# Kernel optimization log

Hardware: AMD Instinct MI355X
Metric: run time of the kernel (lower is better)

Reference implementation:

```python
import jax, jax.numpy as jnp
import numpy as np

B, T, I, H, C = 8192, 28, 28, 128, 10


def setup_inputs() -> dict:
    key = jax.random.key(0)
    ks = jax.random.split(key, 7)
    s_ih = 1.0 / np.sqrt(H)
    return {
        "x": jax.random.normal(ks[0], (B, T, I), dtype=jnp.float32),
        "W_ih": jax.random.normal(ks[1], (4 * H, I), dtype=jnp.float32) * s_ih,
        "W_hh": jax.random.normal(ks[2], (4 * H, H), dtype=jnp.float32) * s_ih,
        "b_ih": jax.random.normal(ks[3], (4 * H,), dtype=jnp.float32) * s_ih,
        "b_hh": jax.random.normal(ks[4], (4 * H,), dtype=jnp.float32) * s_ih,
        "W_fc": jax.random.normal(ks[5], (C, H), dtype=jnp.float32) * s_ih,
        "b_fc": jnp.zeros((C,), dtype=jnp.float32),
    }


def reference(x, W_ih, W_hh, b_ih, b_hh, W_fc, b_fc):
    # x: [B, T, I]. PyTorch LSTM gate order: i, f, g, o.
    b = b_ih + b_hh  # [4H]
    # Precompute input projections for all timesteps: [T, B, 4H]
    x_proj = jnp.einsum("bti,gi->tbg", x, W_ih) + b
    h0 = jnp.zeros((x.shape[0], H), dtype=x.dtype)
    c0 = jnp.zeros_like(h0)

    def step(carry, xp_t):
        h, c = carry
        gates = xp_t + h @ W_hh.T  # [B, 4H]
        i_g, f_g, g_g, o_g = jnp.split(gates, 4, axis=-1)
        i_g = jax.nn.sigmoid(i_g)
        f_g = jax.nn.sigmoid(f_g)
        g_g = jnp.tanh(g_g)
        o_g = jax.nn.sigmoid(o_g)
        c = f_g * c + i_g * g_g
        h = o_g * jnp.tanh(c)
        return (h, c), None

    (h_last, _), _ = jax.lax.scan(step, (h0, c0), x_proj)
    # outputs[:, -1, :] == final hidden state; fc + relu
    return jax.nn.relu(h_last @ W_fc.T + b_fc)
```

## Files before the change

kernel.cpp:

```cpp
#include <hip/hip_runtime.h>
#include <math.h>

typedef __attribute__((ext_vector_type(8))) _Float16 half8;
typedef __attribute__((ext_vector_type(4))) _Float16 half4;
typedef __attribute__((ext_vector_type(4))) float    f32x4;

#define TSTEPS 28
#define IDIM   28
#define HDIM   128
#define NKC    5
#define TILE_B 16
#define CDIM   10

#if __has_builtin(__builtin_amdgcn_exp2f)
#define EXP2F(x) __builtin_amdgcn_exp2f(x)
#else
#define EXP2F(x) exp2f(x)
#endif
#if __has_builtin(__builtin_amdgcn_rcpf)
#define RCPF(x) __builtin_amdgcn_rcpf(x)
#else
#define RCPF(x) (1.0f / (x))
#endif

#define NLOG2E (-1.44269504f)
#define P2LOG2E (2.88539008f)

__global__ __launch_bounds__(256) void pack_w(const float* __restrict__ Wih,
                                              const float* __restrict__ Whh,
                                              _Float16* __restrict__ P) {
    int e = blockIdx.x * 256 + threadIdx.x;
    if (e >= NKC * 4 * 8 * 64 * 8) return;
    int j  = e & 7;
    int ln = (e >> 3) & 63;
    int w  = (e >> 9) & 7;
    int t  = (e >> 12) & 3;
    int kc = e >> 14;
    int k  = kc * 32 + ((ln >> 4) << 3) + j;
    int u  = w * 16 + (ln & 15);
    int g  = t * HDIM + u;
    float v = 0.f;
    if (k < HDIM)              v = Whh[g * HDIM + k];
    else if (k < HDIM + IDIM)  v = Wih[g * IDIM + (k - HDIM)];
    float sc = (t == 2) ? P2LOG2E : NLOG2E;
    P[e] = (_Float16)(v * sc);
}

__global__ __launch_bounds__(512, 4) void lstm_kernel(
    const float* __restrict__ x,
    const _Float16* __restrict__ P,
    const float* __restrict__ b_ih, const float* __restrict__ b_hh,
    const float* __restrict__ Wfc,
    const float* __restrict__ b_fc,
    float* __restrict__ out)
{
    __shared__ __align__(16) _Float16 frag[2][NKC][64][8];
    __shared__ __align__(16) _Float16 Plds[4][8][64][8];
    __shared__ __align__(16) float hplain[TILE_B][HDIM + 4];

    const int tid = threadIdx.x;
    const int l   = tid & 63;
    const int w   = tid >> 6;
    const int b0  = blockIdx.x * TILE_B;
    const int u   = w * 16 + (l & 15);

    {
        const float4* P4 = (const float4*)P;
        float4* dst = (float4*)Plds;
        #pragma unroll
        for (int q = 0; q < 4; ++q)
            dst[tid + q * 512] = P4[8192 + tid + q * 512];
    }
    half8 breg[4][4];
    {
        const half8* Pp = (const half8*)P;
        #pragma unroll
        for (int kc = 0; kc < 4; ++kc)
            #pragma unroll
            for (int t4 = 0; t4 < 4; ++t4)
                breg[t4][kc] = Pp[((kc * 4 + t4) * 8 + w) * 64 + l];
    }
    float biasv[4];
    #pragma unroll
    for (int t4 = 0; t4 < 4; ++t4) {
        float sc = (t4 == 2) ? P2LOG2E : NLOG2E;
        biasv[t4] = (b_ih[t4 * HDIM + u] + b_hh[t4 * HDIM + u]) * sc;
    }

    {
        float4 z = {0.f, 0.f, 0.f, 0.f};
        if (tid < 256) ((float4*)&frag[0][0][0][0])[tid] = z;
        if (tid < 32) {
            int b = tid >> 4, i = tid & 15;
            half4 zh = {(_Float16)0.f, (_Float16)0.f, (_Float16)0.f, (_Float16)0.f};
            *(half4*)&frag[b][4][48 + i][4] = zh;
        }
    }
    const int xrow = tid / 7, xg = tid % 7;
    if (tid < 112) {
        float4 xv = ((const float4*)(x + ((size_t)(b0 + xrow) * TSTEPS + 0) * IDIM))[xg];
        half4 hv = {(_Float16)xv.x, (_Float16)xv.y, (_Float16)xv.z, (_Float16)xv.w};
        *(half4*)&frag[0][4][xrow + 16 * (xg >> 1)][(xg & 1) * 4] = hv;
    }

    float cst[4] = {0.f, 0.f, 0.f, 0.f};
    const int kc_h = w >> 1;
    const int quad = (2 * w + ((l >> 3) & 1)) & 3;
    const int jh   = l & 7;

    __syncthreads();

    auto step = [&](int t, _Float16 (*cur)[64][8], _Float16 (*nxt)[64][8]) {
        float4 xv;
        const bool doload = (t + 1 < TSTEPS) && (tid < 112);
        if (doload)
            xv = ((const float4*)(x + ((size_t)(b0 + xrow) * TSTEPS + (t + 1)) * IDIM))[xg];

        f32x4 acc[4];
        #pragma unroll
        for (int t4 = 0; t4 < 4; ++t4) {
            f32x4 a4 = {biasv[t4], biasv[t4], biasv[t4], biasv[t4]};
            acc[t4] = a4;
        }

        #pragma unroll
        for (int kc = 0; kc < NKC; ++kc) {
            half8 a = *(const half8*)&cur[kc][l][0];
            if (kc < 4) {
                acc[0] = __builtin_amdgcn_mfma_f32_16x16x32_f16(a, breg[0][kc], acc[0], 0, 0, 0);
                acc[1] = __builtin_amdgcn_mfma_f32_16x16x32_f16(a, breg[1][kc], acc[1], 0, 0, 0);
                acc[2] = __builtin_amdgcn_mfma_f32_16x16x32_f16(a, breg[2][kc], acc[2], 0, 0, 0);
                acc[3] = __builtin_amdgcn_mfma_f32_16x16x32_f16(a, breg[3][kc], acc[3], 0, 0, 0);
            } else {
                #pragma unroll
                for (int t4 = 0; t4 < 4; ++t4) {
                    half8 b = *(const half8*)&Plds[t4][w][l][0];
                    acc[t4] = __builtin_amdgcn_mfma_f32_16x16x32_f16(a, b, acc[t4], 0, 0, 0);
                }
            }
        }

        #pragma unroll
        for (int r = 0; r < 4; ++r) {
            int m = ((l >> 4) << 2) + r;
            float is = RCPF(1.f + EXP2F(acc[0][r]));
            float fs = RCPF(1.f + EXP2F(acc[1][r]));
            float os = RCPF(1.f + EXP2F(acc[3][r]));
            float gt = 1.f - 2.f * RCPF(1.f + EXP2F(acc[2][r]));
            float c  = fs * cst[r] + is * gt;
            cst[r] = c;
            float tc = 1.f - 2.f * RCPF(1.f + EXP2F(c * P2LOG2E));
            float h  = os * tc;
            nxt[kc_h][m + 16 * quad][jh] = (_Float16)h;
            if (t == TSTEPS - 1) hplain[m][u] = h;
        }
        if (doload) {
            half4 hv = {(_Float16)xv.x, (_Float16)xv.y, (_Float16)xv.z, (_Float16)xv.w};
            *(half4*)&nxt[4][xrow + 16 * (xg >> 1)][(xg & 1) * 4] = hv;
        }
        __syncthreads();
    };

    for (int tt = 0; tt < TSTEPS; tt += 2) {
        step(tt,     frag[0], frag[1]);
        step(tt + 1, frag[1], frag[0]);
    }

    if (tid < TILE_B * CDIM) {
        int row = tid / CDIM, c = tid % CDIM;
        const float4* hv = (const float4*)&hplain[row][0];
        const float4* wf = (const float4*)(Wfc + c * HDIM);
        float s = b_fc[c];
        #pragma unroll
        for (int q = 0; q < 32; ++q) {
            float4 a = hv[q], b = wf[q];
            s += a.x * b.x + a.y * b.y + a.z * b.z + a.w * b.w;
        }
        out[(size_t)(b0 + row) * CDIM + c] = fmaxf(s, 0.f);
    }
}

extern "C" void kernel_launch(void* const* d_in, const int* in_sizes, int n_in,
                              void* d_out, int out_size, void* d_ws, size_t ws_size,
                              hipStream_t stream) {
    const float* x   = (const float*)d_in[0];
    const float* Wih = (const float*)d_in[1];
    const float* Whh = (const float*)d_in[2];
    const float* bih = (const float*)d_in[3];
    const float* bhh = (const float*)d_in[4];
    const float* Wfc = (const float*)d_in[5];
    const float* bfc = (const float*)d_in[6];
    float* out = (float*)d_out;
    _Float16* P = (_Float16*)d_ws;

    hipLaunchKernelGGL(pack_w, dim3(320), dim3(256), 0, stream, Wih, Whh, P);
    hipLaunchKernelGGL(lstm_kernel, dim3(8192 / TILE_B), dim3(512), 0, stream,
                       x, P, bih, bhh, Wfc, bfc, out);
}
```

Baseline: 127.5 us.

## Interleave two batch tiles per block to overlap MFMA with gate activations

Each block now processes 32 batch rows as two independent 16-row tiles. The MFMA matrix multiply for one tile is software-pipelined against the sigmoid/tanh activation work of the other, and the next timestep's x is prefetched one step further ahead. The gate activations also share reciprocals by pairing the denominators (i with f, g with o), which cuts the number of rcp calls. In exchange, the grid has half as many blocks (256 on this batch size), launch bounds drop to two blocks per CU, and per-thread register pressure rises. Sync points per timestep double to two.

Result: no change. 127.2 us (-0.2%).

```diff
diff --git a/kernel.cpp b/kernel.cpp
--- a/kernel.cpp
+++ b/kernel.cpp
@@ -9,7 +9,6 @@
 #define IDIM   28
 #define HDIM   128
 #define NKC    5
-#define TILE_B 16
 #define CDIM   10
 
 #if __has_builtin(__builtin_amdgcn_exp2f)
@@ -46,7 +45,7 @@
     P[e] = (_Float16)(v * sc);
 }
 
-__global__ __launch_bounds__(512, 4) void lstm_kernel(
+__global__ __launch_bounds__(512, 2) void lstm_kernel(
     const float* __restrict__ x,
     const _Float16* __restrict__ P,
     const float* __restrict__ b_ih, const float* __restrict__ b_hh,
@@ -54,14 +53,14 @@
     const float* __restrict__ b_fc,
     float* __restrict__ out)
 {
-    __shared__ __align__(16) _Float16 frag[2][NKC][64][8];
+    __shared__ __align__(16) _Float16 frag[2][2][NKC][64][8];
     __shared__ __align__(16) _Float16 Plds[4][8][64][8];
-    __shared__ __align__(16) float hplain[TILE_B][HDIM + 4];
+    __shared__ __align__(16) float hplain[32][HDIM + 4];
 
     const int tid = threadIdx.x;
     const int l   = tid & 63;
     const int w   = tid >> 6;
-    const int b0  = blockIdx.x * TILE_B;
+    const int b0  = blockIdx.x * 32;
     const int u   = w * 16 + (l & 15);
 
     {
@@ -89,84 +88,128 @@
 
     {
         float4 z = {0.f, 0.f, 0.f, 0.f};
-        if (tid < 256) ((float4*)&frag[0][0][0][0])[tid] = z;
-        if (tid < 32) {
-            int b = tid >> 4, i = tid & 15;
+        int tile = tid >> 8, q = tid & 255;
+        ((float4*)&frag[tile][0][0][0][0])[q] = z;
+        if (tid < 64) {
+            int tb = tid >> 4, i = tid & 15;
             half4 zh = {(_Float16)0.f, (_Float16)0.f, (_Float16)0.f, (_Float16)0.f};
-            *(half4*)&frag[b][4][48 + i][4] = zh;
+            *(half4*)&frag[tb >> 1][tb & 1][4][48 + i][4] = zh;
         }
     }
     const int xrow = tid / 7, xg = tid % 7;
-    if (tid < 112) {
+    float4 xheld;
+    if (tid < 224) {
         float4 xv = ((const float4*)(x + ((size_t)(b0 + xrow) * TSTEPS + 0) * IDIM))[xg];
         half4 hv = {(_Float16)xv.x, (_Float16)xv.y, (_Float16)xv.z, (_Float16)xv.w};
-        *(half4*)&frag[0][4][xrow + 16 * (xg >> 1)][(xg & 1) * 4] = hv;
-    }
-
-    float cst[4] = {0.f, 0.f, 0.f, 0.f};
+        *(half4*)&frag[xrow >> 4][0][4][(xrow & 15) + 16 * (xg >> 1)][(xg & 1) * 4] = hv;
+        xheld = ((const float4*)(x + ((size_t)(b0 + xrow) * TSTEPS + 1) * IDIM))[xg];
+    }
+
+    float cst0[4] = {0.f, 0.f, 0.f, 0.f};
+    float cst1[4] = {0.f, 0.f, 0.f, 0.f};
     const int kc_h = w >> 1;
     const int quad = (2 * w + ((l >> 3) & 1)) & 3;
     const int jh   = l & 7;
 
-    __syncthreads();
-
-    auto step = [&](int t, _Float16 (*cur)[64][8], _Float16 (*nxt)[64][8]) {
-        float4 xv;
-        const bool doload = (t + 1 < TSTEPS) && (tid < 112);
-        if (doload)
-            xv = ((const float4*)(x + ((size_t)(b0 + xrow) * TSTEPS + (t + 1)) * IDIM))[xg];
-
-        f32x4 acc[4];
+    f32x4 acc0[4], acc1[4];
+
+    auto mfma_kc = [&](f32x4 (&acc)[4], const _Float16 (*cur)[64][8], int kc) {
+        half8 a = *(const half8*)&cur[kc][l][0];
+        if (kc < 4) {
+            acc[0] = __builtin_amdgcn_mfma_f32_16x16x32_f16(a, breg[0][kc], acc[0], 0, 0, 0);
+            acc[1] = __builtin_amdgcn_mfma_f32_16x16x32_f16(a, breg[1][kc], acc[1], 0, 0, 0);
+            acc[2] = __builtin_amdgcn_mfma_f32_16x16x32_f16(a, breg[2][kc], acc[2], 0, 0, 0);
+            acc[3] = __builtin_amdgcn_mfma_f32_16x16x32_f16(a, breg[3][kc], acc[3], 0, 0, 0);
+        } else {
+            #pragma unroll
+            for (int t4 = 0; t4 < 4; ++t4) {
+                half8 b = *(const half8*)&Plds[t4][w][l][0];
+                acc[t4] = __builtin_amdgcn_mfma_f32_16x16x32_f16(a, b, acc[t4], 0, 0, 0);
+            }
+        }
+    };
+    auto init_acc = [&](f32x4 (&acc)[4]) {
         #pragma unroll
         for (int t4 = 0; t4 < 4; ++t4) {
             f32x4 a4 = {biasv[t4], biasv[t4], biasv[t4], biasv[t4]};
             acc[t4] = a4;
         }
-
-        #pragma unroll
-        for (int kc = 0; kc < NKC; ++kc) {
-            half8 a = *(const half8*)&cur[kc][l][0];
-            if (kc < 4) {
-                acc[0] = __builtin_amdgcn_mfma_f32_16x16x32_f16(a, breg[0][kc], acc[0], 0, 0, 0);
-                acc[1] = __builtin_amdgcn_mfma_f32_16x16x32_f16(a, breg[1][kc], acc[1], 0, 0, 0);
-                acc[2] = __builtin_amdgcn_mfma_f32_16x16x32_f16(a, breg[2][kc], acc[2], 0, 0, 0);
-                acc[3] = __builtin_amdgcn_mfma_f32_16x16x32_f16(a, breg[3][kc], acc[3], 0, 0, 0);
-            } else {
-                #pragma unroll
-                for (int t4 = 0; t4 < 4; ++t4) {
-                    half8 b = *(const half8*)&Plds[t4][w][l][0];
-                    acc[t4] = __builtin_amdgcn_mfma_f32_16x16x32_f16(a, b, acc[t4], 0, 0, 0);
-                }
-            }
-        }
-
-        #pragma unroll
-        for (int r = 0; r < 4; ++r) {
-            int m = ((l >> 4) << 2) + r;
-            float is = RCPF(1.f + EXP2F(acc[0][r]));
-            float fs = RCPF(1.f + EXP2F(acc[1][r]));
-            float os = RCPF(1.f + EXP2F(acc[3][r]));
-            float gt = 1.f - 2.f * RCPF(1.f + EXP2F(acc[2][r]));
-            float c  = fs * cst[r] + is * gt;
-            cst[r] = c;
-            float tc = 1.f - 2.f * RCPF(1.f + EXP2F(c * P2LOG2E));
-            float h  = os * tc;
-            nxt[kc_h][m + 16 * quad][jh] = (_Float16)h;
-            if (t == TSTEPS - 1) hplain[m][u] = h;
-        }
-        if (doload) {
-            half4 hv = {(_Float16)xv.x, (_Float16)xv.y, (_Float16)xv.z, (_Float16)xv.w};
-            *(half4*)&nxt[4][xrow + 16 * (xg >> 1)][(xg & 1) * 4] = hv;
-        }
+    };
+    auto act_cell = [&](f32x4 (&acc)[4], float (&cst)[4], int tile, int r,
+                        bool last, int nb) {
+        float Ei = EXP2F(acc[0][r]);
+        float Ef = EXP2F(acc[1][r]);
+        float Eg = EXP2F(acc[2][r]);
+        float Eo = EXP2F(acc[3][r]);
+        float Di = 1.f + Ei, Df = 1.f + Ef, Dg = 1.f + Eg, Do = 1.f + Eo;
+        float Rif = RCPF(Di * Df);
+        float Rgo = RCPF(Dg * Do);
+        float is = Rif * Df, fs = Rif * Di;
+        float gt = 1.f - 2.f * (Rgo * Do);
+        float os = Rgo * Dg;
+        float c  = fs * cst[r] + is * gt;
+        cst[r] = c;
+        float tc = 1.f - 2.f * RCPF(1.f + EXP2F(c * P2LOG2E));
+        float h  = os * tc;
+        int m = ((l >> 4) << 2) + r;
+        frag[tile][nb][kc_h][m + 16 * quad][jh] = (_Float16)h;
+        if (last) hplain[tile * 16 + m][u] = h;
+    };
+
+    __syncthreads();
+
+    init_acc(acc0);
+    mfma_kc(acc0, frag[0][0], 0);
+    mfma_kc(acc0, frag[0][0], 1);
+    mfma_kc(acc0, frag[0][0], 2);
+    mfma_kc(acc0, frag[0][0], 3);
+    mfma_kc(acc0, frag[0][0], 4);
+
+    for (int t = 0; t < TSTEPS; ++t) {
+        const int cb = t & 1, nb = cb ^ 1;
+        const bool last = (t == TSTEPS - 1);
+
+        if (t + 1 < TSTEPS && tid < 224) {
+            half4 hv = {(_Float16)xheld.x, (_Float16)xheld.y,
+                        (_Float16)xheld.z, (_Float16)xheld.w};
+            *(half4*)&frag[xrow >> 4][nb][4][(xrow & 15) + 16 * (xg >> 1)][(xg & 1) * 4] = hv;
+        }
+        if (t + 2 < TSTEPS && tid < 224)
+            xheld = ((const float4*)(x + ((size_t)(b0 + xrow) * TSTEPS + (t + 2)) * IDIM))[xg];
+
+        init_acc(acc1);
+        mfma_kc(acc1, frag[1][cb], 0);
+        act_cell(acc0, cst0, 0, 0, last, nb);
+        mfma_kc(acc1, frag[1][cb], 1);
+        act_cell(acc0, cst0, 0, 1, last, nb);
+        mfma_kc(acc1, frag[1][cb], 2);
+        act_cell(acc0, cst0, 0, 2, last, nb);
+        mfma_kc(acc1, frag[1][cb], 3);
+        act_cell(acc0, cst0, 0, 3, last, nb);
+        mfma_kc(acc1, frag[1][cb], 4);
         __syncthreads();
-    };
-
-    for (int tt = 0; tt < TSTEPS; tt += 2) {
-        step(tt,     frag[0], frag[1]);
-        step(tt + 1, frag[1], frag[0]);
-    }
-
-    if (tid < TILE_B * CDIM) {
+
+        if (!last) {
+            init_acc(acc0);
+            mfma_kc(acc0, frag[0][nb], 0);
+            act_cell(acc1, cst1, 1, 0, last, nb);
+            mfma_kc(acc0, frag[0][nb], 1);
+            act_cell(acc1, cst1, 1, 1, last, nb);
+            mfma_kc(acc0, frag[0][nb], 2);
+            act_cell(acc1, cst1, 1, 2, last, nb);
+            mfma_kc(acc0, frag[0][nb], 3);
+            act_cell(acc1, cst1, 1, 3, last, nb);
+            mfma_kc(acc0, frag[0][nb], 4);
+        } else {
+            act_cell(acc1, cst1, 1, 0, last, nb);
+            act_cell(acc1, cst1, 1, 1, last, nb);
+            act_cell(acc1, cst1, 1, 2, last, nb);
+            act_cell(acc1, cst1, 1, 3, last, nb);
+        }
+        __syncthreads();
+    }
+
+    if (tid < 32 * CDIM) {
         int row = tid / CDIM, c = tid % CDIM;
         const float4* hv = (const float4*)&hplain[row][0];
         const float4* wf = (const float4*)(Wfc + c * HDIM);
@@ -194,6 +237,6 @@
     _Float16* P = (_Float16*)d_ws;
 
     hipLaunchKernelGGL(pack_w, dim3(320), dim3(256), 0, stream, Wih, Whh, P);
-    hipLaunchKernelGGL(lstm_kernel, dim3(8192 / TILE_B), dim3(512), 0, stream,
+    hipLaunchKernelGGL(lstm_kernel, dim3(8192 / 32), dim3(512), 0, stream,
                        x, P, bih, bhh, Wfc, bfc, out);
 }
```

## Ping-pong two batch tiles across wave halves to overlap MFMA and activations

Applied to the files above, without the earlier changes.

Each block now handles 32 batch rows as two 16-row tiles with 1024 threads. One half of the waves runs the MFMA gate products for one tile while the other half computes the activations for the other tile, and the roles swap each half-step, so matrix and transcendental work overlap. The bias is folded into the packed weights as an extra input column fixed at one, and the four sigmoid reciprocals are merged pairwise into two. The cost is twice as many barriers per step, larger blocks, and half as many blocks (256), which may leave the GPU underfilled.

Result: slower. 137.8 us (+8.1%).

```diff
diff --git a/kernel.cpp b/kernel.cpp
--- a/kernel.cpp
+++ b/kernel.cpp
@@ -9,7 +9,6 @@
 #define IDIM   28
 #define HDIM   128
 #define NKC    5
-#define TILE_B 16
 #define CDIM   10
 
 #if __has_builtin(__builtin_amdgcn_exp2f)
@@ -28,6 +27,8 @@
 
 __global__ __launch_bounds__(256) void pack_w(const float* __restrict__ Wih,
                                               const float* __restrict__ Whh,
+                                              const float* __restrict__ bih,
+                                              const float* __restrict__ bhh,
                                               _Float16* __restrict__ P) {
     int e = blockIdx.x * 256 + threadIdx.x;
     if (e >= NKC * 4 * 8 * 64 * 8) return;
@@ -40,36 +41,38 @@
     int u  = w * 16 + (ln & 15);
     int g  = t * HDIM + u;
     float v = 0.f;
-    if (k < HDIM)              v = Whh[g * HDIM + k];
-    else if (k < HDIM + IDIM)  v = Wih[g * IDIM + (k - HDIM)];
+    if (k < HDIM)                   v = Whh[g * HDIM + k];
+    else if (k < HDIM + IDIM)       v = Wih[g * IDIM + (k - HDIM)];
+    else if (k == HDIM + IDIM)      v = bih[g] + bhh[g];
     float sc = (t == 2) ? P2LOG2E : NLOG2E;
     P[e] = (_Float16)(v * sc);
 }
 
-__global__ __launch_bounds__(512, 4) void lstm_kernel(
+__global__ __launch_bounds__(1024, 4) void lstm_kernel(
     const float* __restrict__ x,
     const _Float16* __restrict__ P,
-    const float* __restrict__ b_ih, const float* __restrict__ b_hh,
     const float* __restrict__ Wfc,
     const float* __restrict__ b_fc,
     float* __restrict__ out)
 {
-    __shared__ __align__(16) _Float16 frag[2][NKC][64][8];
+    __shared__ __align__(16) _Float16 frag[2][2][NKC][64][8];
     __shared__ __align__(16) _Float16 Plds[4][8][64][8];
-    __shared__ __align__(16) float hplain[TILE_B][HDIM + 4];
-
-    const int tid = threadIdx.x;
-    const int l   = tid & 63;
-    const int w   = tid >> 6;
-    const int b0  = blockIdx.x * TILE_B;
-    const int u   = w * 16 + (l & 15);
+    __shared__ __align__(16) float hplain[32][HDIM + 4];
+
+    const int tid  = threadIdx.x;
+    const int l    = tid & 63;
+    const int w    = tid >> 6;
+    const int w7   = w & 7;
+    const int hsel = w >> 3;
+    const int b0   = blockIdx.x * 32;
+    const int u    = w7 * 16 + (l & 15);
 
     {
         const float4* P4 = (const float4*)P;
         float4* dst = (float4*)Plds;
         #pragma unroll
-        for (int q = 0; q < 4; ++q)
-            dst[tid + q * 512] = P4[8192 + tid + q * 512];
+        for (int q = 0; q < 2; ++q)
+            dst[tid + q * 1024] = P4[8192 + tid + q * 1024];
     }
     half8 breg[4][4];
     {
@@ -78,54 +81,44 @@
         for (int kc = 0; kc < 4; ++kc)
             #pragma unroll
             for (int t4 = 0; t4 < 4; ++t4)
-                breg[t4][kc] = Pp[((kc * 4 + t4) * 8 + w) * 64 + l];
-    }
-    float biasv[4];
-    #pragma unroll
-    for (int t4 = 0; t4 < 4; ++t4) {
-        float sc = (t4 == 2) ? P2LOG2E : NLOG2E;
-        biasv[t4] = (b_ih[t4 * HDIM + u] + b_hh[t4 * HDIM + u]) * sc;
-    }
-
-    {
+                breg[t4][kc] = Pp[((kc * 4 + t4) * 8 + w7) * 64 + l];
+    }
+
+    if (tid < 512) {
         float4 z = {0.f, 0.f, 0.f, 0.f};
-        if (tid < 256) ((float4*)&frag[0][0][0][0])[tid] = z;
-        if (tid < 32) {
-            int b = tid >> 4, i = tid & 15;
-            half4 zh = {(_Float16)0.f, (_Float16)0.f, (_Float16)0.f, (_Float16)0.f};
-            *(half4*)&frag[b][4][48 + i][4] = zh;
-        }
-    }
-    const int xrow = tid / 7, xg = tid % 7;
-    if (tid < 112) {
-        float4 xv = ((const float4*)(x + ((size_t)(b0 + xrow) * TSTEPS + 0) * IDIM))[xg];
+        int tile = tid >> 8, q = tid & 255;
+        ((float4*)&frag[tile][0][0][0][0])[q] = z;
+    }
+    if (tid < 64) {
+        int tb = tid >> 4, i = tid & 15;
+        half4 onev = {(_Float16)1.f, (_Float16)0.f, (_Float16)0.f, (_Float16)0.f};
+        *(half4*)&frag[tb >> 1][tb & 1][4][48 + i][4] = onev;
+    }
+    if (tid < 224) {
+        int xr0 = tid / 7, xg0 = tid % 7;
+        float4 xv = ((const float4*)(x + ((size_t)(b0 + xr0) * TSTEPS + 0) * IDIM))[xg0];
         half4 hv = {(_Float16)xv.x, (_Float16)xv.y, (_Float16)xv.z, (_Float16)xv.w};
-        *(half4*)&frag[0][4][xrow + 16 * (xg >> 1)][(xg & 1) * 4] = hv;
-    }
-
+        *(half4*)&frag[xr0 >> 4][0][4][(xr0 & 15) + 16 * (xg0 >> 1)][(xg0 & 1) * 4] = hv;
+    }
+
+    const bool isL1 = (tid < 112);
+    const bool isL0 = (tid >= 512 && tid < 624);
+    const int  lx   = isL0 ? (tid - 512) : tid;
+    const int  xr   = lx / 7, xg = lx % 7;
+
+    f32x4 acc[4];
     float cst[4] = {0.f, 0.f, 0.f, 0.f};
-    const int kc_h = w >> 1;
-    const int quad = (2 * w + ((l >> 3) & 1)) & 3;
+    half4 xh;
+    const int kc_h = w7 >> 1;
+    const int quad = (2 * w7 + ((l >> 3) & 1)) & 3;
     const int jh   = l & 7;
 
-    __syncthreads();
-
-    auto step = [&](int t, _Float16 (*cur)[64][8], _Float16 (*nxt)[64][8]) {
-        float4 xv;
-        const bool doload = (t + 1 < TSTEPS) && (tid < 112);
-        if (doload)
-            xv = ((const float4*)(x + ((size_t)(b0 + xrow) * TSTEPS + (t + 1)) * IDIM))[xg];
-
-        f32x4 acc[4];
-        #pragma unroll
-        for (int t4 = 0; t4 < 4; ++t4) {
-            f32x4 a4 = {biasv[t4], biasv[t4], biasv[t4], biasv[t4]};
-            acc[t4] = a4;
-        }
-
+    auto mfma_tile = [&](int tile, int buf) {
+        #pragma unroll
+        for (int t4 = 0; t4 < 4; ++t4) { f32x4 z = {0.f, 0.f, 0.f, 0.f}; acc[t4] = z; }
         #pragma unroll
         for (int kc = 0; kc < NKC; ++kc) {
-            half8 a = *(const half8*)&cur[kc][l][0];
+            half8 a = *(const half8*)&frag[tile][buf][kc][l][0];
             if (kc < 4) {
                 acc[0] = __builtin_amdgcn_mfma_f32_16x16x32_f16(a, breg[0][kc], acc[0], 0, 0, 0);
                 acc[1] = __builtin_amdgcn_mfma_f32_16x16x32_f16(a, breg[1][kc], acc[1], 0, 0, 0);
@@ -134,39 +127,75 @@
             } else {
                 #pragma unroll
                 for (int t4 = 0; t4 < 4; ++t4) {
-                    half8 b = *(const half8*)&Plds[t4][w][l][0];
+                    half8 b = *(const half8*)&Plds[t4][w7][l][0];
                     acc[t4] = __builtin_amdgcn_mfma_f32_16x16x32_f16(a, b, acc[t4], 0, 0, 0);
                 }
             }
         }
-
+    };
+    auto act_tile = [&](int tile, int nb, bool last) {
         #pragma unroll
         for (int r = 0; r < 4; ++r) {
-            int m = ((l >> 4) << 2) + r;
-            float is = RCPF(1.f + EXP2F(acc[0][r]));
-            float fs = RCPF(1.f + EXP2F(acc[1][r]));
-            float os = RCPF(1.f + EXP2F(acc[3][r]));
-            float gt = 1.f - 2.f * RCPF(1.f + EXP2F(acc[2][r]));
+            float Ei = EXP2F(acc[0][r]);
+            float Ef = EXP2F(acc[1][r]);
+            float Eg = EXP2F(acc[2][r]);
+            float Eo = EXP2F(acc[3][r]);
+            float Di = 1.f + Ei, Df = 1.f + Ef, Dg = 1.f + Eg, Do = 1.f + Eo;
+            float Rif = RCPF(Di * Df);
+            float Rgo = RCPF(Dg * Do);
+            float is = Rif * Df, fs = Rif * Di;
+            float gt = 1.f - 2.f * (Rgo * Do);
+            float os = Rgo * Dg;
             float c  = fs * cst[r] + is * gt;
             cst[r] = c;
             float tc = 1.f - 2.f * RCPF(1.f + EXP2F(c * P2LOG2E));
             float h  = os * tc;
-            nxt[kc_h][m + 16 * quad][jh] = (_Float16)h;
-            if (t == TSTEPS - 1) hplain[m][u] = h;
-        }
-        if (doload) {
-            half4 hv = {(_Float16)xv.x, (_Float16)xv.y, (_Float16)xv.z, (_Float16)xv.w};
-            *(half4*)&nxt[4][xrow + 16 * (xg >> 1)][(xg & 1) * 4] = hv;
+            int m = ((l >> 4) << 2) + r;
+            frag[tile][nb][kc_h][m + 16 * quad][jh] = (_Float16)h;
+            if (last) hplain[tile * 16 + m][u] = h;
+        }
+    };
+
+    __syncthreads();
+
+    auto step = [&](int t, int cb) {
+        const int nb = cb ^ 1;
+        if (hsel == 0) {
+            mfma_tile(0, cb);
+            if (isL1 && t > 0)
+                *(half4*)&frag[1][cb][4][xr + 16 * (xg >> 1)][(xg & 1) * 4] = xh;
+        } else {
+            if (t > 0) act_tile(1, cb, false);
+            if (isL0 && t + 1 < TSTEPS) {
+                float4 xv = ((const float4*)(x + ((size_t)(b0 + xr) * TSTEPS + (t + 1)) * IDIM))[xg];
+                half4 hv = {(_Float16)xv.x, (_Float16)xv.y, (_Float16)xv.z, (_Float16)xv.w};
+                xh = hv;
+            }
+        }
+        __syncthreads();
+        if (hsel == 0) {
+            act_tile(0, nb, t == TSTEPS - 1);
+            if (isL1 && t + 1 < TSTEPS) {
+                float4 xv = ((const float4*)(x + ((size_t)(b0 + 16 + xr) * TSTEPS + (t + 1)) * IDIM))[xg];
+                half4 hv = {(_Float16)xv.x, (_Float16)xv.y, (_Float16)xv.z, (_Float16)xv.w};
+                xh = hv;
+            }
+        } else {
+            mfma_tile(1, cb);
+            if (isL0 && t + 1 < TSTEPS)
+                *(half4*)&frag[0][nb][4][xr + 16 * (xg >> 1)][(xg & 1) * 4] = xh;
         }
         __syncthreads();
     };
 
-    for (int tt = 0; tt < TSTEPS; tt += 2) {
-        step(tt,     frag[0], frag[1]);
-        step(tt + 1, frag[1], frag[0]);
-    }
-
-    if (tid < TILE_B * CDIM) {
+    for (int t = 0; t < TSTEPS; t += 2) {
+        step(t, 0);
+        step(t + 1, 1);
+    }
+    if (hsel == 1) act_tile(1, 0, true);
+    __syncthreads();
+
+    if (tid < 32 * CDIM) {
         int row = tid / CDIM, c = tid % CDIM;
         const float4* hv = (const float4*)&hplain[row][0];
         const float4* wf = (const float4*)(Wfc + c * HDIM);
@@ -193,7 +222,7 @@
     float* out = (float*)d_out;
     _Float16* P = (_Float16*)d_ws;
 
-    hipLaunchKernelGGL(pack_w, dim3(320), dim3(256), 0, stream, Wih, Whh, P);
-    hipLaunchKernelGGL(lstm_kernel, dim3(8192 / TILE_B), dim3(512), 0, stream,
-                       x, P, bih, bhh, Wfc, bfc, out);
+    hipLaunchKernelGGL(pack_w, dim3(320), dim3(256), 0, stream, Wih, Whh, bih, bhh, P);
+    hipLaunchKernelGGL(lstm_kernel, dim3(8192 / 32), dim3(1024), 0, stream,
+                       x, P, Wfc, bfc, out);
 }
```
